# Kernel optimization log

Measured on AMD Instinct MI355X. Metric: run time of the kernel, lower is better.

Reference implementation:

```python
import jax, jax.numpy as jnp
import numpy as np

RADIUS = 0.3
GRID_MIN, GRID_MAX, NUM = -1.5, 1.5, 5
H = (GRID_MAX - GRID_MIN) / (NUM - 1)  # hat-basis width = 0.75
M, N, HID = 4096, 1024, 8


def hat_basis(x):
    # x: [...]; returns [..., NUM] linear B-spline (hat) basis values
    grid = jnp.linspace(GRID_MIN, GRID_MAX, NUM, dtype=x.dtype)
    return jax.nn.relu(1.0 - jnp.abs(x[..., None] - grid) / H)


def cubic_window(dist):
    q = dist / RADIUS
    w = 1.0 - 6.0 * q**2 + 8.0 * q**3 - 3.0 * q**4
    return jnp.where(q <= 1.0, w, 0.0)


def setup_inputs() -> dict:
    key = jax.random.key(0)
    k1, k2, k3, k4, k5, k6 = jax.random.split(key, 6)
    x = jax.random.uniform(k1, (M, 2), jnp.float32, -1.0, 1.0)
    nodes = jax.random.uniform(k2, (N, 2), jnp.float32, -1.0, 1.0)
    W1a = jax.random.normal(k3, (HID, NUM), jnp.float32) * 0.3
    W1b = jax.random.normal(k4, (HID, NUM), jnp.float32) * 0.3
    W2 = jax.random.normal(k5, (1, HID * NUM), jnp.float32) * 0.3
    w = jax.random.normal(k6, (N, 1), jnp.float32)
    return {"x": x, "nodes": nodes, "W1a": W1a, "W1b": W1b, "W2": W2, "w": w}


def reference(x, nodes, W1a, W1b, W2, w):
    # pairwise diff / distance: [M, N, 2], [M, N]
    diff = x[:, None, :] - nodes[None, :, :]
    dist = jnp.linalg.norm(diff, axis=2)
    kin = diff / RADIUS                      # KAN input, [M, N, 2]

    # KAN layer 1: per-input-dim hat basis -> small GEMM, summed
    basis_in = hat_basis(kin)                # [M, N, 2, NUM]
    W1 = jnp.stack([W1a, W1b], axis=0)       # [2, HID, NUM]
    hidden = jnp.einsum('mnis,ihs->mnh', basis_in, W1)  # [M, N, HID]

    # KAN layer 2: hat basis of hidden -> [M, N]
    basis_h = hat_basis(hidden)              # [M, N, HID, NUM]
    phi_raw = jnp.einsum('mnhs,hs->mn', basis_h, W2.reshape(HID, NUM))

    # window, normalize, weighted reduction
    phi_win = phi_raw * cubic_window(dist)   # [M, N]
    phi = phi_win / (jnp.sum(phi_win, axis=1, keepdims=True) + 1e-10)
    u = phi @ w                              # [M, 1]
    return u
```

## Files before the change

kernel.cpp:

```cpp
#include <hip/hip_runtime.h>

#define M_PTS 4096
#define N_NODES 1024
#define WAVES 16
#define CAP 128

#define INV_R (1.0f / 0.3f)
#define R2 (0.3f * 0.3f)
#define INV_H (4.0f / 3.0f)

__global__ __launch_bounds__(1024) void kan_meshfree_kernel(
    const float* __restrict__ x,
    const float* __restrict__ nodes,
    const float* __restrict__ W1a,
    const float* __restrict__ W1b,
    const float* __restrict__ W2,
    const float* __restrict__ w,
    float* __restrict__ u)
{
    __shared__ float4 s_c[WAVES][CAP];
    __shared__ float2 s_T1a[4][8];
    __shared__ float2 s_T1b[4][8];
    __shared__ float2 s_T2[7][9];

    const int tid = threadIdx.x;
    const int wave = tid >> 6;
    const int lane = tid & 63;
    const int m = blockIdx.x * WAVES + wave;

    if (tid < 32) {
        const int j = tid >> 3, h = tid & 7;
        const float a0 = W1a[h * 5 + j], a1 = W1a[h * 5 + j + 1];
        s_T1a[j][h] = make_float2(a0, a1 - a0);
        const float b0 = W1b[h * 5 + j], b1 = W1b[h * 5 + j + 1];
        s_T1b[j][h] = make_float2(b0, b1 - b0);
    } else if (tid < 32 + 56) {
        const int t = tid - 32;
        const int k = t >> 3, h = t & 7;
        const float q0 = (k >= 1 && k <= 5) ? W2[h * 5 + k - 1] : 0.f;
        const float q1 = (k + 1 <= 5) ? W2[h * 5 + k] : 0.f;
        s_T2[k][h] = make_float2(q0, q1 - q0);
    }

    const float2 xm = ((const float2*)x)[m];
    const float4* __restrict__ nodes4 = (const float4*)nodes;
    const unsigned long long lmask = (1ull << lane) - 1ull;

    int cnt = 0;
#pragma unroll
    for (int base = 0; base < N_NODES / 2; base += 64) {
        const int p = base + lane;
        const float4 nd = nodes4[p];
        const float d0a = xm.x - nd.x, d1a = xm.y - nd.y;
        const float d0b = xm.x - nd.z, d1b = xm.y - nd.w;
        const bool actA = fmaf(d0a, d0a, d1a * d1a) <= R2;
        const bool actB = fmaf(d0b, d0b, d1b * d1b) <= R2;
        const unsigned long long mA = __ballot(actA);
        if (actA) {
            const int pos = cnt + __popcll(mA & lmask);
            if (pos < CAP) s_c[wave][pos] = make_float4(d0a, d1a, __int_as_float(2 * p), 0.f);
        }
        cnt += __popcll(mA);
        const unsigned long long mB = __ballot(actB);
        if (actB) {
            const int pos = cnt + __popcll(mB & lmask);
            if (pos < CAP) s_c[wave][pos] = make_float4(d0b, d1b, __int_as_float(2 * p + 1), 0.f);
        }
        cnt += __popcll(mB);
    }
    if (cnt > CAP) cnt = CAP;

    __syncthreads();

    float S1 = 0.f, S2 = 0.f;
    for (int i = lane; i < cnt; i += 64) {
        const float4 c = s_c[wave][i];
        const float wn = w[__float_as_int(c.z)];
        const float d0 = c.x, d1 = c.y;
        const float dist2 = fmaf(d0, d0, d1 * d1);
        const float q2 = dist2 * (INV_R * INV_R);
        const float q = __builtin_amdgcn_sqrtf(q2);
        const float win = fmaf(q2, fmaf(q, fmaf(-3.f, q, 8.f), -6.f), 1.f);

        const float ta = fmaf(d0 * INV_R, INV_H, 2.f);
        const float tb = fmaf(d1 * INV_R, INV_H, 2.f);
        const float fja = floorf(ta), fjb = floorf(tb);
        const float fa = ta - fja, fb = tb - fjb;
        const int ja = (int)fja, jb = (int)fjb;
        const float2* __restrict__ rowA = s_T1a[ja];
        const float2* __restrict__ rowB = s_T1b[jb];

        float phi = 0.f;
#pragma unroll
        for (int h = 0; h < 8; ++h) {
            const float2 A = rowA[h];
            const float2 B = rowB[h];
            const float hid = fmaf(fa, A.y, A.x) + fmaf(fb, B.y, B.x);
            float t2 = fmaf(hid, INV_H, 3.f);
            t2 = fminf(fmaxf(t2, 0.f), 6.f);
            const float fj2 = floorf(t2);
            const float f2 = t2 - fj2;
            const int j2 = (int)fj2;
            const float2 C = s_T2[j2][h];
            phi += fmaf(f2, C.y, C.x);
        }

        const float pw = phi * win;
        S1 += pw;
        S2 = fmaf(pw, wn, S2);
    }

#pragma unroll
    for (int off = 32; off >= 1; off >>= 1) {
        S1 += __shfl_down(S1, off);
        S2 += __shfl_down(S2, off);
    }

    if (lane == 0) u[m] = S2 / (S1 + 1e-10f);
}

extern "C" void kernel_launch(void* const* d_in, const int* in_sizes, int n_in,
                              void* d_out, int out_size, void* d_ws, size_t ws_size,
                              hipStream_t stream) {
    const float* x     = (const float*)d_in[0];
    const float* nodes = (const float*)d_in[1];
    const float* W1a   = (const float*)d_in[2];
    const float* W1b   = (const float*)d_in[3];
    const float* W2    = (const float*)d_in[4];
    const float* w     = (const float*)d_in[5];
    float* u = (float*)d_out;

    dim3 grid(M_PTS / WAVES);
    dim3 block(64 * WAVES);
    hipLaunchKernelGGL(kan_meshfree_kernel, grid, block, 0, stream,
                       x, nodes, W1a, W1b, W2, w, u);
}
```

Baseline: 10.42 us.

## Replicate weight tables per wave and drop block barrier; fixed two-slot body

Each wave now builds its own private copy of the KAN weight tables in shared memory, so the block-wide __syncthreads is replaced by a wave-local LDS waitcnt. The per-lane candidate loop becomes a fixed two-slot evaluation (lane and lane+64), with invalid slots zeroed and masked, which removes loop control and lets both bodies overlap. This costs more LDS and redundant table construction per wave, and relies on wave-synchronous execution for correctness.

```diff
diff --git a/kernel.cpp b/kernel.cpp
--- a/kernel.cpp
+++ b/kernel.cpp
@@ -19,27 +19,27 @@
     float* __restrict__ u)
 {
     __shared__ float4 s_c[WAVES][CAP];
-    __shared__ float2 s_T1a[4][8];
-    __shared__ float2 s_T1b[4][8];
-    __shared__ float2 s_T2[7][9];
+    __shared__ float2 s_T1a[WAVES][4][8];
+    __shared__ float2 s_T1b[WAVES][4][8];
+    __shared__ float2 s_T2[WAVES][7][9];
 
     const int tid = threadIdx.x;
     const int wave = tid >> 6;
     const int lane = tid & 63;
     const int m = blockIdx.x * WAVES + wave;
 
-    if (tid < 32) {
-        const int j = tid >> 3, h = tid & 7;
+    if (lane < 32) {
+        const int j = lane >> 3, h = lane & 7;
         const float a0 = W1a[h * 5 + j], a1 = W1a[h * 5 + j + 1];
-        s_T1a[j][h] = make_float2(a0, a1 - a0);
+        s_T1a[wave][j][h] = make_float2(a0, a1 - a0);
         const float b0 = W1b[h * 5 + j], b1 = W1b[h * 5 + j + 1];
-        s_T1b[j][h] = make_float2(b0, b1 - b0);
-    } else if (tid < 32 + 56) {
-        const int t = tid - 32;
-        const int k = t >> 3, h = t & 7;
+        s_T1b[wave][j][h] = make_float2(b0, b1 - b0);
+    }
+    if (lane < 56) {
+        const int k = lane >> 3, h = lane & 7;
         const float q0 = (k >= 1 && k <= 5) ? W2[h * 5 + k - 1] : 0.f;
-        const float q1 = (k + 1 <= 5) ? W2[h * 5 + k] : 0.f;
-        s_T2[k][h] = make_float2(q0, q1 - q0);
+        const float q1 = (k <= 4) ? W2[h * 5 + k] : 0.f;
+        s_T2[wave][k][h] = make_float2(q0, q1 - q0);
     }
 
     const float2 xm = ((const float2*)x)[m];
@@ -70,12 +70,17 @@
     }
     if (cnt > CAP) cnt = CAP;
 
-    __syncthreads();
+    asm volatile("s_waitcnt lgkmcnt(0)" ::: "memory");
 
-    float S1 = 0.f, S2 = 0.f;
-    for (int i = lane; i < cnt; i += 64) {
-        const float4 c = s_c[wave][i];
-        const float wn = w[__float_as_int(c.z)];
+    const bool v0 = lane < cnt;
+    const bool v1 = lane + 64 < cnt;
+    const float4 z4 = make_float4(0.f, 0.f, 0.f, 0.f);
+    const float4 c0 = v0 ? s_c[wave][lane] : z4;
+    const float4 c1 = v1 ? s_c[wave][lane + 64] : z4;
+    const float wn0 = w[__float_as_int(c0.z)];
+    const float wn1 = w[__float_as_int(c1.z)];
+
+    auto body = [&](const float4 c) -> float {
         const float d0 = c.x, d1 = c.y;
         const float dist2 = fmaf(d0, d0, d1 * d1);
         const float q2 = dist2 * (INV_R * INV_R);
@@ -87,8 +92,8 @@
         const float fja = floorf(ta), fjb = floorf(tb);
         const float fa = ta - fja, fb = tb - fjb;
         const int ja = (int)fja, jb = (int)fjb;
-        const float2* __restrict__ rowA = s_T1a[ja];
-        const float2* __restrict__ rowB = s_T1b[jb];
+        const float2* __restrict__ rowA = s_T1a[wave][ja];
+        const float2* __restrict__ rowB = s_T1b[wave][jb];
 
         float phi = 0.f;
 #pragma unroll
@@ -101,14 +106,18 @@
             const float fj2 = floorf(t2);
             const float f2 = t2 - fj2;
             const int j2 = (int)fj2;
-            const float2 C = s_T2[j2][h];
+            const float2 C = s_T2[wave][j2][h];
             phi += fmaf(f2, C.y, C.x);
         }
+        return phi * win;
+    };
 
-        const float pw = phi * win;
-        S1 += pw;
-        S2 = fmaf(pw, wn, S2);
-    }
+    const float pw0 = body(c0);
+    const float pw1 = body(c1);
+
+    float S1 = 0.f, S2 = 0.f;
+    if (v0) { S1 += pw0; S2 = fmaf(pw0, wn0, S2); }
+    if (v1) { S1 += pw1; S2 = fmaf(pw1, wn1, S2); }
 
 #pragma unroll
     for (int off = 32; off >= 1; off >>= 1) {
```

Result: slower. 10.84 us (+4.0%).
